# Performance work log

Hardware: AMD Instinct MI355X
Metric: run time of the kernel (lower is better)

The kernel has to match this reference:

```python
import jax, jax.numpy as jnp
import numpy as np

# torch grid_sample semantics: grid[...,0] indexes width, grid[...,1] height, grid[...,2] depth;
# align_corners=True -> idx = (g+1)/2*(size-1); padding_mode='zeros' -> out-of-range taps contribute 0.

def _bilinear(plane, gx, gy):
    # plane: (C,H,W); gx,gy: (P,) in [-1,1]. Returns (P,C).
    C, H, W = plane.shape
    ix = (gx + 1.0) * 0.5 * (W - 1)
    iy = (gy + 1.0) * 0.5 * (H - 1)
    x0 = jnp.floor(ix); y0 = jnp.floor(iy)
    wx = ix - x0; wy = iy - y0
    x0i = x0.astype(jnp.int32); x1i = x0i + 1
    y0i = y0.astype(jnp.int32); y1i = y0i + 1
    def tap(xi, yi):
        valid = ((xi >= 0) & (xi < W) & (yi >= 0) & (yi < H)).astype(plane.dtype)
        v = plane[:, jnp.clip(yi, 0, H - 1), jnp.clip(xi, 0, W - 1)]  # (C,P)
        return v * valid
    out = (tap(x0i, y0i) * ((1 - wx) * (1 - wy)) + tap(x1i, y0i) * (wx * (1 - wy))
         + tap(x0i, y1i) * ((1 - wx) * wy)      + tap(x1i, y1i) * (wx * wy))
    return out.T  # (P,C)


def _trilinear(vol, gx, gy, gz):
    # vol: (C,D,H,W); gx->W, gy->H, gz->D. Returns (P,C).
    C, D, H, W = vol.shape
    ix = (gx + 1.0) * 0.5 * (W - 1)
    iy = (gy + 1.0) * 0.5 * (H - 1)
    iz = (gz + 1.0) * 0.5 * (D - 1)
    x0 = jnp.floor(ix); y0 = jnp.floor(iy); z0 = jnp.floor(iz)
    wx = ix - x0; wy = iy - y0; wz = iz - z0
    x0i = x0.astype(jnp.int32); y0i = y0.astype(jnp.int32); z0i = z0.astype(jnp.int32)
    def tap(xi, yi, zi):
        valid = ((xi >= 0) & (xi < W) & (yi >= 0) & (yi < H) & (zi >= 0) & (zi < D)).astype(vol.dtype)
        v = vol[:, jnp.clip(zi, 0, D - 1), jnp.clip(yi, 0, H - 1), jnp.clip(xi, 0, W - 1)]
        return v * valid
    out = jnp.zeros((C, gx.shape[0]), vol.dtype)
    for dz, wz_ in ((0, 1 - wz), (1, wz)):
        for dy, wy_ in ((0, 1 - wy), (1, wy)):
            for dx, wx_ in ((0, 1 - wx), (1, wx)):
                out = out + tap(x0i + dx, y0i + dy, z0i + dz) * (wx_ * wy_ * wz_)
    return out.T


def setup_inputs() -> dict:
    key = jax.random.key(0)
    ks = jax.random.split(key, 16)
    P, Cp, Np_, Cl, Nl, Cv, Nv = 262144, 32, 128, 64, 128, 16, 64
    s = 0.001
    d = {
        'coordinates': jax.random.uniform(ks[0], (1, P, 3), jnp.float32, -1.0, 1.0),
        'plane_xy': jax.random.normal(ks[1], (Cp, Np_, Np_)) * s,
        'plane_yz': jax.random.normal(ks[2], (Cp, Np_, Np_)) * s,
        'plane_xz': jax.random.normal(ks[3], (Cp, Np_, Np_)) * s,
        'plane_xy_g': jax.random.normal(ks[4], (Cp, Np_, Np_)) * s,
        'plane_yz_g': jax.random.normal(ks[5], (Cp, Np_, Np_)) * s,
        'plane_xz_g': jax.random.normal(ks[6], (Cp, Np_, Np_)) * s,
        'line_x': jax.random.normal(ks[7], (Cl, Nl, 1)) * s,
        'line_y': jax.random.normal(ks[8], (Cl, Nl, 1)) * s,
        'line_z': jax.random.normal(ks[9], (Cl, Nl, 1)) * s,
        'line_x_g': jax.random.normal(ks[10], (Cl, Nl, 1)) * s,
        'line_y_g': jax.random.normal(ks[11], (Cl, Nl, 1)) * s,
        'line_z_g': jax.random.normal(ks[12], (Cl, Nl, 1)) * s,
        'volume': jax.random.normal(ks[13], (Cv, Nv, Nv, Nv)) * s,
        'volume_g': jax.random.normal(ks[14], (Cv, Nv, Nv, Nv)) * s,
    }
    return d


def reference(coordinates, plane_xy, plane_yz, plane_xz, plane_xy_g, plane_yz_g, plane_xz_g,
              line_x, line_y, line_z, line_x_g, line_y_g, line_z_g, volume, volume_g):
    c = coordinates[0]  # (P,3), batch squeezed as in torch .squeeze(0)
    x, y, z = c[:, 0], c[:, 1], c[:, 2]
    zero = jnp.zeros_like(x)
    # Planes: coords2d (a,b) -> grid x=a (width), grid y=b (height).
    xy_e = _bilinear(plane_xy, x, y); xy_g = _bilinear(plane_xy_g, x, y)
    yz_e = _bilinear(plane_yz, y, z); yz_g = _bilinear(plane_yz_g, y, z)
    xz_e = _bilinear(plane_xz, x, z); xz_g = _bilinear(plane_xz_g, x, z)
    feats = jnp.sum(xy_e * (xy_g >= 0) + yz_e * (yz_g >= 0) + xz_e * (xz_g >= 0), axis=-1)
    # Lines: grid pair is (coord, 0) -> coord indexes the singleton width dim (faithful to torch).
    x_e = _bilinear(line_x, x, zero); x_g = _bilinear(line_x_g, x, zero)
    y_e = _bilinear(line_y, y, zero); y_g = _bilinear(line_y_g, y, zero)
    z_e = _bilinear(line_z, z, zero); z_g = _bilinear(line_z_g, z, zero)
    line_feats = jnp.sum(x_e * (x_g >= 0) + y_e * (y_g >= 0) + z_e * (z_g >= 0), axis=-1)
    # Volume: grid (x,y,z) -> x:W, y:H, z:D.
    v_e = _trilinear(volume, x, y, z); v_g = _trilinear(volume_g, x, y, z)
    vol_feats = jnp.sum(v_e * (v_g >= 0), axis=-1)
    return feats + line_feats + vol_feats  # (P,)
```

## Files before the change

### kernel.cpp

```cpp
#include <hip/hip_runtime.h>
#include <hip/hip_bf16.h>

#pragma clang fp contract(off)

typedef unsigned short u16;
typedef unsigned int u32;
typedef __attribute__((ext_vector_type(4))) float f32x4;
typedef __attribute__((ext_vector_type(8))) unsigned short u16x8;
typedef __attribute__((ext_vector_type(4))) unsigned short u16x4;

__device__ __forceinline__ float bf2f(u16 u) {
    union { unsigned int i; float f; } v; v.i = ((unsigned int)u) << 16; return v.f;
}
__device__ __forceinline__ u16 f2bf(float f) {
    __hip_bfloat16 h = __float2bfloat16(f);
    return *(u16*)&h;
}

__device__ __forceinline__ int cell_of(float x, float y, float z)
{
    int cx = (int)fminf(fmaxf((x + 1.0f) * 4.0f, 0.0f), 7.0f);
    int cy = (int)fminf(fmaxf((y + 1.0f) * 4.0f, 0.0f), 7.0f);
    int cz = (int)fminf(fmaxf((z + 1.0f) * 4.0f, 0.0f), 7.0f);
    return cx + (cy << 3) + (cz << 6);
}

__global__ __launch_bounds__(256) void fused_prep_count(
    const float* __restrict__ pxy, const float* __restrict__ pxyg,
    const float* __restrict__ pyz, const float* __restrict__ pyzg,
    const float* __restrict__ pxz, const float* __restrict__ pxzg,
    const float* __restrict__ vol, const float* __restrict__ volg,
    char* __restrict__ tpxy, char* __restrict__ tpyz, char* __restrict__ tpxz,
    char* __restrict__ tv,
    const float* __restrict__ coords, u32* __restrict__ hist, int P)
{
    __shared__ float smem[4160];
    const int b = blockIdx.x;
    const int t = threadIdx.x;

    if (b < 768) {
        int which = b >> 8, blk = b & 255;
        const float* e = (which == 0) ? pxy  : (which == 1) ? pyz  : pxz;
        const float* g = (which == 0) ? pxyg : (which == 1) ? pyzg : pxzg;
        char* dst      = (which == 0) ? tpxy : (which == 1) ? tpyz : tpxz;
        const int tbase = blk * 64;
#pragma unroll
        for (int i = 0; i < 16; ++i) {
            int eidx = i * 256 + t;
            int c  = eidx >> 6;
            int pl = eidx & 63;
            const float* src = (c < 32) ? e : g;
            int cs = (c < 32) ? c : (c - 32);
            smem[c * 65 + pl] = src[(size_t)cs * 16384 + tbase + pl];
        }
        __syncthreads();
#pragma unroll
        for (int i = 0; i < 3; ++i) {
            int sid = i * 256 + t;
            int rec = sid / 12;
            int seg = sid % 12;
            char* outp = dst + (size_t)(tbase + rec) * 192 + seg * 16;
            if (seg < 4) {
                u16x8 pk;
#pragma unroll
                for (int k = 0; k < 8; ++k) pk[k] = f2bf(smem[(seg * 8 + k) * 65 + rec]);
                *(u16x8*)outp = pk;
            } else {
                f32x4 pk;
#pragma unroll
                for (int k = 0; k < 4; ++k) pk[k] = smem[(32 + (seg - 4) * 4 + k) * 65 + rec];
                *(f32x4*)outp = pk;
            }
        }
    } else if (b < 2816) {
        int blk = b - 768;
        const int tbase = blk * 128;
#pragma unroll
        for (int i = 0; i < 16; ++i) {
            int eidx = i * 256 + t;
            int c  = eidx >> 7;
            int pl = eidx & 127;
            const float* src = (c < 16) ? vol : volg;
            int cs = (c < 16) ? c : (c - 16);
            smem[c * 129 + pl] = src[(size_t)cs * 262144 + tbase + pl];
        }
        __syncthreads();
#pragma unroll
        for (int i = 0; i < 3; ++i) {
            int sid = i * 256 + t;
            int rec = sid / 6;
            int seg = sid % 6;
            char* outp = tv + (size_t)(tbase + rec) * 96 + seg * 16;
            if (seg < 2) {
                u16x8 pk;
#pragma unroll
                for (int k = 0; k < 8; ++k) pk[k] = f2bf(smem[(seg * 8 + k) * 129 + rec]);
                *(u16x8*)outp = pk;
            } else {
                f32x4 pk;
#pragma unroll
                for (int k = 0; k < 4; ++k) pk[k] = smem[(16 + (seg - 2) * 4 + k) * 129 + rec];
                *(f32x4*)outp = pk;
            }
        }
    } else {
        u32* h = (u32*)smem;
        int blk = b - 2816;
        h[t] = 0u; h[t + 256] = 0u;
        __syncthreads();
        int p = blk * 256 + t;
        if (p < P) {
            float x = coords[3 * p + 0];
            float y = coords[3 * p + 1];
            float z = coords[3 * p + 2];
            atomicAdd(&h[cell_of(x, y, z)], 1u);
        }
        __syncthreads();
        u32* hb = hist + (size_t)blk * 512;
        hb[t] = h[t];
        hb[t + 256] = h[t + 256];
    }
}

__global__ __launch_bounds__(256) void cell_base(
    const u32* __restrict__ hist, u32* __restrict__ base,
    u32* __restrict__ totals, int nb)
{
    int c = blockIdx.x;
    int t = threadIdx.x;
    int b0 = t * 4;
    u32 v[4];
#pragma unroll
    for (int i = 0; i < 4; ++i)
        v[i] = (b0 + i < nb) ? hist[(size_t)(b0 + i) * 512 + c] : 0u;
    u32 lsum = v[0] + v[1] + v[2] + v[3];
    __shared__ u32 ls[256];
    ls[t] = lsum;
    __syncthreads();
#pragma unroll
    for (int off = 1; off < 256; off <<= 1) {
        u32 x = (t >= off) ? ls[t - off] : 0u;
        __syncthreads();
        ls[t] += x;
        __syncthreads();
    }
    u32 acc = ls[t] - lsum;
#pragma unroll
    for (int i = 0; i < 4; ++i) {
        if (b0 + i < nb) base[(size_t)(b0 + i) * 512 + c] = acc;
        acc += v[i];
    }
    if (t == 255) totals[c] = acc;
}

__global__ __launch_bounds__(256) void bucket_scatter2(
    const float* __restrict__ coords, const u32* __restrict__ base,
    const u32* __restrict__ totals, u32* __restrict__ perm, int P)
{
    __shared__ u32 lh[512];
    __shared__ u32 ts[512];
    __shared__ u32 torig[512];
    int t = threadIdx.x;
    lh[t] = 0u; lh[t + 256] = 0u;
    u32 a0 = totals[t], a1 = totals[t + 256];
    ts[t] = a0; ts[t + 256] = a1;
    torig[t] = a0; torig[t + 256] = a1;
    __syncthreads();
#pragma unroll
    for (int off = 1; off < 512; off <<= 1) {
        u32 x0 = (t >= off) ? ts[t - off] : 0u;
        u32 x1 = (t + 256 >= off) ? ts[t + 256 - off] : 0u;
        __syncthreads();
        ts[t] += x0; ts[t + 256] += x1;
        __syncthreads();
    }
    ts[t]       -= torig[t];
    ts[t + 256] -= torig[t + 256];
    __syncthreads();

    int p = blockIdx.x * 256 + t;
    if (p < P) {
        float x = coords[3 * p + 0];
        float y = coords[3 * p + 1];
        float z = coords[3 * p + 2];
        int cell = cell_of(x, y, z);
        u32 rank = atomicAdd(&lh[cell], 1u);
        u32 pos = ts[cell] + base[(size_t)blockIdx.x * 512 + cell] + rank;
        perm[pos] = (u32)p;
    }
}

__device__ __forceinline__ float plane_lane(
    const char* __restrict__ tp, float gx, float gy, int s)
{
    float ix = fminf(fmaxf((gx + 1.0f) * 0.5f * 127.0f, 0.0f), 127.0f);
    float iy = fminf(fmaxf((gy + 1.0f) * 0.5f * 127.0f, 0.0f), 127.0f);
    float x0f = floorf(ix), y0f = floorf(iy);
    float wx = ix - x0f, wy = iy - y0f;
    int x0 = (int)x0f, y0 = (int)y0f;
    int x1 = x0 + 1, y1 = y0 + 1;
    float vx1 = (x1 < 128) ? 1.0f : 0.0f;
    float vy1 = (y1 < 128) ? 1.0f : 0.0f;
    int x1c = min(x1, 127), y1c = min(y1, 127);
    float omwx = 1.0f - wx, omwy = 1.0f - wy;
    float ws4[4];
    ws4[0] = omwx * omwy;
    ws4[1] = (wx * omwy) * vx1;
    ws4[2] = (omwx * wy) * vy1;
    ws4[3] = ((wx * wy) * vx1) * vy1;
    unsigned o[4];
    o[0] = (unsigned)(y0  * 128 + x0 ) * 192u;
    o[1] = (unsigned)(y0  * 128 + x1c) * 192u;
    o[2] = (unsigned)(y1c * 128 + x0 ) * 192u;
    o[3] = (unsigned)(y1c * 128 + x1c) * 192u;

    const int eoff = s * 16;
    const int goff = 64 + s * 32;
    f32x4 ea0 = {0.0f, 0.0f, 0.0f, 0.0f}, ea1 = {0.0f, 0.0f, 0.0f, 0.0f};
    f32x4 ga0 = {0.0f, 0.0f, 0.0f, 0.0f}, ga1 = {0.0f, 0.0f, 0.0f, 0.0f};
#pragma unroll
    for (int t = 0; t < 4; ++t) {
        const char* bp = tp + o[t];
        float w = ws4[t];
        u16x8 ev = *(const u16x8*)(bp + eoff);
        f32x4 g0 = *(const f32x4*)(bp + goff);
        f32x4 g1 = *(const f32x4*)(bp + goff + 16);
#pragma unroll
        for (int j = 0; j < 4; ++j) {
            ga0[j] = ga0[j] + g0[j] * w;
            ga1[j] = ga1[j] + g1[j] * w;
            ea0[j] = fmaf(bf2f(ev[j]), w, ea0[j]);
            ea1[j] = fmaf(bf2f(ev[j + 4]), w, ea1[j]);
        }
    }
    float acc = 0.0f;
#pragma unroll
    for (int j = 0; j < 4; ++j) {
        acc += (ga0[j] >= 0.0f) ? ea0[j] : 0.0f;
        acc += (ga1[j] >= 0.0f) ? ea1[j] : 0.0f;
    }
    return acc;
}

__device__ __forceinline__ float vol_lane(
    const char* __restrict__ tv, float gx, float gy, float gz, int s)
{
    float ix = fminf(fmaxf((gx + 1.0f) * 0.5f * 63.0f, 0.0f), 63.0f);
    float iy = fminf(fmaxf((gy + 1.0f) * 0.5f * 63.0f, 0.0f), 63.0f);
    float iz = fminf(fmaxf((gz + 1.0f) * 0.5f * 63.0f, 0.0f), 63.0f);
    float x0f = floorf(ix), y0f = floorf(iy), z0f = floorf(iz);
    float wx = ix - x0f, wy = iy - y0f, wz = iz - z0f;
    int x0 = (int)x0f, y0 = (int)y0f, z0 = (int)z0f;
    int x1 = x0 + 1, y1 = y0 + 1, z1 = z0 + 1;
    float fx[2] = {1.0f - wx, wx}, fy[2] = {1.0f - wy, wy}, fz[2] = {1.0f - wz, wz};
    float vx[2] = {1.0f, (x1 < 64) ? 1.0f : 0.0f};
    float vy[2] = {1.0f, (y1 < 64) ? 1.0f : 0.0f};
    float vz[2] = {1.0f, (z1 < 64) ? 1.0f : 0.0f};
    int xi[2] = {x0, min(x1, 63)}, yi[2] = {y0, min(y1, 63)}, zi[2] = {z0, min(z1, 63)};

    unsigned off[8];
    float w[8];
#pragma unroll
    for (int dz = 0; dz < 2; ++dz)
#pragma unroll
        for (int dy = 0; dy < 2; ++dy)
#pragma unroll
            for (int dx = 0; dx < 2; ++dx) {
                int tt = (dz << 2) | (dy << 1) | dx;
                w[tt] = (((fx[dx] * fy[dy]) * fz[dz]) * vx[dx]) * (vy[dy] * vz[dz]);
                off[tt] = (unsigned)((zi[dz] * 64 + yi[dy]) * 64 + xi[dx]) * 96u;
            }
    const int eoff = s * 8;
    const int goff = 32 + s * 16;
    f32x4 ea = {0.0f, 0.0f, 0.0f, 0.0f}, ga = {0.0f, 0.0f, 0.0f, 0.0f};
#pragma unroll
    for (int tt = 0; tt < 8; ++tt) {
        const char* bp = tv + off[tt];
        float wt = w[tt];
        u16x4 ev = *(const u16x4*)(bp + eoff);
        f32x4 gv = *(const f32x4*)(bp + goff);
#pragma unroll
        for (int j = 0; j < 4; ++j) {
            ga[j] = ga[j] + gv[j] * wt;
            ea[j] = fmaf(bf2f(ev[j]), wt, ea[j]);
        }
    }
    float acc = 0.0f;
#pragma unroll
    for (int j = 0; j < 4; ++j)
        acc += (ga[j] >= 0.0f) ? ea[j] : 0.0f;
    return acc;
}

__device__ __forceinline__ float line_pair(const float* __restrict__ e,
                                           const float* __restrict__ g, int c)
{
    float ev = e[c * 128 + 63] * 0.5f + e[c * 128 + 64] * 0.5f;
    float gv = g[c * 128 + 63] * 0.5f + g[c * 128 + 64] * 0.5f;
    return (gv >= 0.0f) ? ev : 0.0f;
}

__device__ __forceinline__ float block_line_const(
    const float* lx, const float* ly, const float* lz,
    const float* lxg, const float* lyg, const float* lzg)
{
    __shared__ float lc_sh;
    int t = threadIdx.x;
    if (t < 64) {
        float part = line_pair(lx, lxg, t) + line_pair(ly, lyg, t) + line_pair(lz, lzg, t);
#pragma unroll
        for (int off = 32; off > 0; off >>= 1) part += __shfl_down(part, off);
        if (t == 0) lc_sh = part;
    }
    __syncthreads();
    return lc_sh;
}

__global__ __launch_bounds__(256) void ctri_main_L(
    const float* __restrict__ coords, const u32* __restrict__ perm,
    const float* __restrict__ lx,  const float* __restrict__ ly,  const float* __restrict__ lz,
    const float* __restrict__ lxg, const float* __restrict__ lyg, const float* __restrict__ lzg,
    const char* __restrict__ tpxy, const char* __restrict__ tpyz, const char* __restrict__ tpxz,
    const char* __restrict__ tv,
    float* __restrict__ out, int P, int nblk)
{
    float lc = block_line_const(lx, ly, lz, lxg, lyg, lzg);
    int b = blockIdx.x;
    int cpx = nblk >> 3;
    int swz = (b & 7) * cpx + (b >> 3);
    int i = swz * 64 + (threadIdx.x >> 2);
    int s = threadIdx.x & 3;
    if (i >= P) return;
    int p = (int)perm[i];
    float x = coords[3 * p + 0];
    float y = coords[3 * p + 1];
    float z = coords[3 * p + 2];
    float part = 0.0f;
    part += plane_lane(tpxy, x, y, s);
    part += plane_lane(tpyz, y, z, s);
    part += plane_lane(tpxz, x, z, s);
    part += vol_lane(tv, x, y, z, s);
    part += __shfl_xor(part, 1, 64);
    part += __shfl_xor(part, 2, 64);
    if (s == 0) out[p] = lc + part;
}

__device__ __forceinline__ float sample_plane_pair_D(
    const float* __restrict__ e, const float* __restrict__ g, float gx, float gy)
{
    float ix = fminf(fmaxf((gx + 1.0f) * 0.5f * 127.0f, 0.0f), 127.0f);
    float iy = fminf(fmaxf((gy + 1.0f) * 0.5f * 127.0f, 0.0f), 127.0f);
    float x0f = floorf(ix), y0f = floorf(iy);
    float wx = ix - x0f, wy = iy - y0f;
    int x0 = (int)x0f, y0 = (int)y0f;
    int x1 = x0 + 1, y1 = y0 + 1;
    float vx1 = (x1 < 128) ? 1.0f : 0.0f;
    float vy1 = (y1 < 128) ? 1.0f : 0.0f;
    int x1c = min(x1, 127), y1c = min(y1, 127);
    float omwx = 1.0f - wx, omwy = 1.0f - wy;
    float w00 = omwx * omwy;
    float w10 = (wx * omwy) * vx1;
    float w01 = (omwx * wy) * vy1;
    float w11 = ((wx * wy) * vx1) * vy1;
    int o00 = y0 * 128 + x0, o10 = y0 * 128 + x1c;
    int o01 = y1c * 128 + x0, o11 = y1c * 128 + x1c;
    float acc = 0.0f;
#pragma unroll 4
    for (int c = 0; c < 32; ++c) {
        const float* ec = e + (size_t)c * 16384;
        const float* gc = g + (size_t)c * 16384;
        float ei = ((ec[o00] * w00 + ec[o10] * w10) + ec[o01] * w01) + ec[o11] * w11;
        float gi = ((gc[o00] * w00 + gc[o10] * w10) + gc[o01] * w01) + gc[o11] * w11;
        acc += (gi >= 0.0f) ? ei : 0.0f;
    }
    return acc;
}

__device__ __forceinline__ float sample_volume_D(
    const float* __restrict__ e, const float* __restrict__ g,
    float gx, float gy, float gz)
{
    float ix = fminf(fmaxf((gx + 1.0f) * 0.5f * 63.0f, 0.0f), 63.0f);
    float iy = fminf(fmaxf((gy + 1.0f) * 0.5f * 63.0f, 0.0f), 63.0f);
    float iz = fminf(fmaxf((gz + 1.0f) * 0.5f * 63.0f, 0.0f), 63.0f);
    float x0f = floorf(ix), y0f = floorf(iy), z0f = floorf(iz);
    float wx = ix - x0f, wy = iy - y0f, wz = iz - z0f;
    int x0 = (int)x0f, y0 = (int)y0f, z0 = (int)z0f;
    int x1 = x0 + 1, y1 = y0 + 1, z1 = z0 + 1;
    float fx[2] = {1.0f - wx, wx}, fy[2] = {1.0f - wy, wy}, fz[2] = {1.0f - wz, wz};
    float vx[2] = {1.0f, (x1 < 64) ? 1.0f : 0.0f};
    float vy[2] = {1.0f, (y1 < 64) ? 1.0f : 0.0f};
    float vz[2] = {1.0f, (z1 < 64) ? 1.0f : 0.0f};
    int xi[2] = {x0, min(x1, 63)}, yi[2] = {y0, min(y1, 63)}, zi[2] = {z0, min(z1, 63)};
    int o[8]; float w[8];
#pragma unroll
    for (int dz = 0; dz < 2; ++dz)
#pragma unroll
        for (int dy = 0; dy < 2; ++dy)
#pragma unroll
            for (int dx = 0; dx < 2; ++dx) {
                int tt = (dz << 2) | (dy << 1) | dx;
                w[tt] = (((fx[dx] * fy[dy]) * fz[dz]) * vx[dx]) * (vy[dy] * vz[dz]);
                o[tt] = (zi[dz] * 64 + yi[dy]) * 64 + xi[dx];
            }
    float acc = 0.0f;
#pragma unroll 2
    for (int c = 0; c < 16; ++c) {
        const float* ec = e + (size_t)c * 262144;
        const float* gc = g + (size_t)c * 262144;
        float ei = 0.0f, gi = 0.0f;
#pragma unroll
        for (int tt = 0; tt < 8; ++tt) {
            ei = ei + ec[o[tt]] * w[tt];
            gi = gi + gc[o[tt]] * w[tt];
        }
        acc += (gi >= 0.0f) ? ei : 0.0f;
    }
    return acc;
}

__global__ __launch_bounds__(256) void ctri_main_D(
    const float* __restrict__ coords,
    const float* __restrict__ lx,  const float* __restrict__ ly,  const float* __restrict__ lz,
    const float* __restrict__ lxg, const float* __restrict__ lyg, const float* __restrict__ lzg,
    const float* __restrict__ pxy, const float* __restrict__ pyz, const float* __restrict__ pxz,
    const float* __restrict__ pxyg, const float* __restrict__ pyzg, const float* __restrict__ pxzg,
    const float* __restrict__ vol, const float* __restrict__ volg,
    float* __restrict__ out, int P)
{
    float lc = block_line_const(lx, ly, lz, lxg, lyg, lzg);
    int p = blockIdx.x * blockDim.x + threadIdx.x;
    if (p >= P) return;
    float x = coords[3 * p + 0];
    float y = coords[3 * p + 1];
    float z = coords[3 * p + 2];
    float acc = lc;
    acc += sample_plane_pair_D(pxy, pxyg, x, y);
    acc += sample_plane_pair_D(pyz, pyzg, y, z);
    acc += sample_plane_pair_D(pxz, pxzg, x, z);
    acc += sample_volume_D(vol, volg, x, y, z);
    out[p] = acc;
}

extern "C" void kernel_launch(void* const* d_in, const int* in_sizes, int n_in,
                              void* d_out, int out_size, void* d_ws, size_t ws_size,
                              hipStream_t stream)
{
    (void)n_in; (void)out_size;
    const float* coords = (const float*)d_in[0];
    const float* pxy  = (const float*)d_in[1];
    const float* pyz  = (const float*)d_in[2];
    const float* pxz  = (const float*)d_in[3];
    const float* pxyg = (const float*)d_in[4];
    const float* pyzg = (const float*)d_in[5];
    const float* pxzg = (const float*)d_in[6];
    const float* lx   = (const float*)d_in[7];
    const float* ly   = (const float*)d_in[8];
    const float* lz   = (const float*)d_in[9];
    const float* lxg  = (const float*)d_in[10];
    const float* lyg  = (const float*)d_in[11];
    const float* lzg  = (const float*)d_in[12];
    const float* vol  = (const float*)d_in[13];
    const float* volg = (const float*)d_in[14];
    float* out = (float*)d_out;

    const int P = in_sizes[0] / 3;
    const int pblocks = (P + 255) / 256;
    const size_t planeRec = (size_t)16384 * 192;
    const size_t volRec   = (size_t)262144 * 96;
    const size_t tabBytes = 3 * planeRec + volRec;
    const size_t permBytes = (size_t)P * 4;
    const size_t histBytes = (size_t)pblocks * 512 * 4;
    const size_t need_bytes = tabBytes + permBytes + 2 * histBytes + 512 * 4;

    if (ws_size >= need_bytes) {
        char* tpxy = (char*)d_ws;
        char* tpyz = tpxy + planeRec;
        char* tpxz = tpyz + planeRec;
        char* tv   = tpxz + planeRec;
        u32* perm   = (u32*)(tv + volRec);
        u32* hist   = perm + P;
        u32* base   = hist + (size_t)pblocks * 512;
        u32* totals = base + (size_t)pblocks * 512;

        fused_prep_count<<<2816 + pblocks, 256, 0, stream>>>(
            pxy, pxyg, pyz, pyzg, pxz, pxzg, vol, volg,
            tpxy, tpyz, tpxz, tv, coords, hist, P);
        cell_base<<<512, 256, 0, stream>>>(hist, base, totals, pblocks);
        bucket_scatter2<<<pblocks, 256, 0, stream>>>(coords, base, totals, perm, P);

        const int mblocks = (P * 4 + 255) / 256;
        ctri_main_L<<<mblocks, 256, 0, stream>>>(coords, perm, lx, ly, lz, lxg, lyg, lzg,
                                                 tpxy, tpyz, tpxz, tv, out, P, mblocks);
    } else {
        ctri_main_D<<<pblocks, 256, 0, stream>>>(coords, lx, ly, lz, lxg, lyg, lzg,
                                                 pxy, pyz, pxz, pxyg, pyzg, pxzg,
                                                 vol, volg, out, P);
    }
}
```

Baseline: 191.7 us.

## Process two points per lane group in main kernel and vectorize prep loads

The main sampling kernel now has each 4-lane group handle two sorted points instead of one, interleaving their plane and volume gathers. This halves the number of blocks and the per-block line-constant reduction overhead, and exposes more memory-level parallelism per thread. The table-prep kernel also switches to 16-byte vector global loads with a padded LDS stride of 68/132 floats instead of scalar loads. The cost is higher register pressure and lower occupancy in the main kernel, plus possible LDS bank conflicts on the transposed reads with the new stride.

Result: faster. 185.8 us (-3.1%).

```diff
diff --git a/kernel.cpp b/kernel.cpp
--- a/kernel.cpp
+++ b/kernel.cpp
@@ -34,7 +34,7 @@
     char* __restrict__ tv,
     const float* __restrict__ coords, u32* __restrict__ hist, int P)
 {
-    __shared__ float smem[4160];
+    __shared__ float smem[4352];
     const int b = blockIdx.x;
     const int t = threadIdx.x;
 
@@ -45,13 +45,14 @@
         char* dst      = (which == 0) ? tpxy : (which == 1) ? tpyz : tpxz;
         const int tbase = blk * 64;
 #pragma unroll
-        for (int i = 0; i < 16; ++i) {
+        for (int i = 0; i < 4; ++i) {
             int eidx = i * 256 + t;
-            int c  = eidx >> 6;
-            int pl = eidx & 63;
+            int c = eidx >> 4;
+            int q = eidx & 15;
             const float* src = (c < 32) ? e : g;
             int cs = (c < 32) ? c : (c - 32);
-            smem[c * 65 + pl] = src[(size_t)cs * 16384 + tbase + pl];
+            f32x4 v = *(const f32x4*)(src + (size_t)cs * 16384 + tbase + q * 4);
+            *(f32x4*)&smem[c * 68 + q * 4] = v;
         }
         __syncthreads();
 #pragma unroll
@@ -63,12 +64,12 @@
             if (seg < 4) {
                 u16x8 pk;
 #pragma unroll
-                for (int k = 0; k < 8; ++k) pk[k] = f2bf(smem[(seg * 8 + k) * 65 + rec]);
+                for (int k = 0; k < 8; ++k) pk[k] = f2bf(smem[(seg * 8 + k) * 68 + rec]);
                 *(u16x8*)outp = pk;
             } else {
                 f32x4 pk;
 #pragma unroll
-                for (int k = 0; k < 4; ++k) pk[k] = smem[(32 + (seg - 4) * 4 + k) * 65 + rec];
+                for (int k = 0; k < 4; ++k) pk[k] = smem[(32 + (seg - 4) * 4 + k) * 68 + rec];
                 *(f32x4*)outp = pk;
             }
         }
@@ -76,13 +77,14 @@
         int blk = b - 768;
         const int tbase = blk * 128;
 #pragma unroll
-        for (int i = 0; i < 16; ++i) {
+        for (int i = 0; i < 4; ++i) {
             int eidx = i * 256 + t;
-            int c  = eidx >> 7;
-            int pl = eidx & 127;
+            int c = eidx >> 5;
+            int q = eidx & 31;
             const float* src = (c < 16) ? vol : volg;
             int cs = (c < 16) ? c : (c - 16);
-            smem[c * 129 + pl] = src[(size_t)cs * 262144 + tbase + pl];
+            f32x4 v = *(const f32x4*)(src + (size_t)cs * 262144 + tbase + q * 4);
+            *(f32x4*)&smem[c * 132 + q * 4] = v;
         }
         __syncthreads();
 #pragma unroll
@@ -94,12 +96,12 @@
             if (seg < 2) {
                 u16x8 pk;
 #pragma unroll
-                for (int k = 0; k < 8; ++k) pk[k] = f2bf(smem[(seg * 8 + k) * 129 + rec]);
+                for (int k = 0; k < 8; ++k) pk[k] = f2bf(smem[(seg * 8 + k) * 132 + rec]);
                 *(u16x8*)outp = pk;
             } else {
                 f32x4 pk;
 #pragma unroll
-                for (int k = 0; k < 4; ++k) pk[k] = smem[(16 + (seg - 2) * 4 + k) * 129 + rec];
+                for (int k = 0; k < 4; ++k) pk[k] = smem[(16 + (seg - 2) * 4 + k) * 132 + rec];
                 *(f32x4*)outp = pk;
             }
         }
@@ -316,7 +318,7 @@
     return lc_sh;
 }
 
-__global__ __launch_bounds__(256) void ctri_main_L(
+__global__ __launch_bounds__(256) void ctri_main_L2(
     const float* __restrict__ coords, const u32* __restrict__ perm,
     const float* __restrict__ lx,  const float* __restrict__ ly,  const float* __restrict__ lz,
     const float* __restrict__ lxg, const float* __restrict__ lyg, const float* __restrict__ lzg,
@@ -328,21 +330,28 @@
     int b = blockIdx.x;
     int cpx = nblk >> 3;
     int swz = (b & 7) * cpx + (b >> 3);
-    int i = swz * 64 + (threadIdx.x >> 2);
+    int g = threadIdx.x >> 2;
     int s = threadIdx.x & 3;
-    if (i >= P) return;
-    int p = (int)perm[i];
-    float x = coords[3 * p + 0];
-    float y = coords[3 * p + 1];
-    float z = coords[3 * p + 2];
-    float part = 0.0f;
-    part += plane_lane(tpxy, x, y, s);
-    part += plane_lane(tpyz, y, z, s);
-    part += plane_lane(tpxz, x, z, s);
-    part += vol_lane(tv, x, y, z, s);
-    part += __shfl_xor(part, 1, 64);
-    part += __shfl_xor(part, 2, 64);
-    if (s == 0) out[p] = lc + part;
+    int i0 = swz * 128 + g * 2;
+    if (i0 >= P) return;
+    int i1 = min(i0 + 1, P - 1);
+    int p0 = (int)perm[i0];
+    int p1 = (int)perm[i1];
+    float x0 = coords[3 * p0 + 0], y0 = coords[3 * p0 + 1], z0 = coords[3 * p0 + 2];
+    float x1 = coords[3 * p1 + 0], y1 = coords[3 * p1 + 1], z1 = coords[3 * p1 + 2];
+    float a0 = 0.0f, a1 = 0.0f;
+    a0 += plane_lane(tpxy, x0, y0, s);   a1 += plane_lane(tpxy, x1, y1, s);
+    a0 += plane_lane(tpyz, y0, z0, s);   a1 += plane_lane(tpyz, y1, z1, s);
+    a0 += plane_lane(tpxz, x0, z0, s);   a1 += plane_lane(tpxz, x1, z1, s);
+    a0 += vol_lane(tv, x0, y0, z0, s);   a1 += vol_lane(tv, x1, y1, z1, s);
+    a0 += __shfl_xor(a0, 1, 64);
+    a0 += __shfl_xor(a0, 2, 64);
+    a1 += __shfl_xor(a1, 1, 64);
+    a1 += __shfl_xor(a1, 2, 64);
+    if (s == 0) {
+        out[p0] = lc + a0;
+        if (i0 + 1 < P) out[p1] = lc + a1;
+    }
 }
 
 __device__ __forceinline__ float sample_plane_pair_D(
@@ -489,9 +498,9 @@
         cell_base<<<512, 256, 0, stream>>>(hist, base, totals, pblocks);
         bucket_scatter2<<<pblocks, 256, 0, stream>>>(coords, base, totals, perm, P);
 
-        const int mblocks = (P * 4 + 255) / 256;
-        ctri_main_L<<<mblocks, 256, 0, stream>>>(coords, perm, lx, ly, lz, lxg, lyg, lzg,
-                                                 tpxy, tpyz, tpxz, tv, out, P, mblocks);
+        const int mblocks = (P * 2 + 255) / 256;
+        ctri_main_L2<<<mblocks, 256, 0, stream>>>(coords, perm, lx, ly, lz, lxg, lyg, lzg,
+                                                  tpxy, tpyz, tpxz, tv, out, P, mblocks);
     } else {
         ctri_main_D<<<pblocks, 256, 0, stream>>>(coords, lx, ly, lz, lxg, lyg, lzg,
                                                  pxy, pyz, pxz, pxyg, pyzg, pxzg,
```
